# Kernel optimization log

Hardware: AMD Instinct MI355X
Metric: run time of the kernel (lower is better)

## Reference

```python
import jax, jax.numpy as jnp
import numpy as np

B = 128; Hm = 13; Wm = 13; P = Hm * Wm; D = 256; TC = 32; RH = 512; EPS = 1e-5
START_TILE = 31


def _ln(x, g, b):
    m = jnp.mean(x, -1, keepdims=True)
    v = jnp.mean((x - m) ** 2, -1, keepdims=True)
    return (x - m) * jax.lax.rsqrt(v + EPS) * g + b


def _gelu(x):
    return jax.nn.gelu(x, approximate=False)


def _fwd(target_map, map_vec, mv_w, mv_b, tile_emb, row_emb, col_emb, pos_w, pos_b,
         c1_w, c1_b, bn1_g, bn1_b, c2_w, c2_b, bn2_g, bn2_b, patch_fc_w, patch_fc_b,
         qkv_w, qkv_b, out_w, out_b, ln1_g, ln1_b, ff1_w, ff1_b, ff2_w, ff2_b,
         ln2_g, ln2_b, gru_wih, gru_whh, gru_bih, gru_bhh,
         fc1_w, fc1_b, fcln_g, fcln_b, fc2_w, fc2_b):
    Bn = map_vec.shape[0]
    ys = jnp.arange(P) // Wm
    xs = jnp.arange(P) % Wm
    d5 = jnp.arange(5)
    # map_vec projection [B,256]
    mv = map_vec @ mv_w.T + mv_b
    # positional embedding for all 169 positions: cat(row_emb[y], col_emb[x]) -> fusion
    pos = jnp.concatenate([row_emb[ys], col_emb[xs]], -1) @ pos_w.T + pos_b  # [P,256]
    # teacher-forced previous tile (use_self_probility=0 path)
    tflat = target_map.reshape(Bn, P)
    prev = jnp.concatenate([jnp.full((Bn, 1), START_TILE, tflat.dtype), tflat[:, :-1]], 1)
    te = tile_emb[prev]  # [B,P,256]
    # 5x5 causal patches: rows y-4..y, cols x-2..x+2, out-of-bounds + current/future-on-row masked
    padded = jnp.pad(target_map, ((0, 0), (4, 0), (2, 2)))  # [B,17,17]
    rows = ys[:, None] + d5
    cols = xs[:, None] + d5
    patch = padded[:, rows[:, :, None], cols[:, None, :]]  # [B,P,5,5]
    vr = (ys[:, None, None] - 4 + d5[None, :, None]) >= 0
    oc = xs[:, None, None] - 2 + d5[None, None, :]
    vc = (oc >= 0) & (oc < Wm)
    mask = (vr & vc)
    mask = mask.at[:, 4, 2:].set(False)  # zero current cell and the two to its right
    patch = jnp.where(mask[None], patch, 0)
    oh = jax.nn.one_hot(patch, TC, dtype=jnp.float32)  # [B,P,row,col,c]
    # torch: permute(0,3,2,1) transposes the spatial dims of the one-hot channels
    ch = jnp.transpose(oh, (0, 1, 4, 3, 2))  # [B,P,32,col,row]
    mch = jnp.broadcast_to(mask.astype(jnp.float32)[None, :, None], (Bn, P, 1, 5, 5))
    x = jnp.concatenate([ch, mch], 2).reshape(Bn * P, TC + 1, 5, 5)
    dn = ('NCHW', 'OIHW', 'NCHW')
    bnsc = 1.0 / np.sqrt(1.0 + EPS)  # eval BN with running mean 0 / var 1
    x = jax.lax.conv_general_dilated(x, c1_w, (1, 1), 'SAME', dimension_numbers=dn) + c1_b[None, :, None, None]
    x = _gelu(x * (bn1_g * bnsc)[None, :, None, None] + bn1_b[None, :, None, None])
    x = jax.lax.conv_general_dilated(x, c2_w, (1, 1), 'VALID', dimension_numbers=dn) + c2_b[None, :, None, None]
    x = _gelu(x * (bn2_g * bnsc)[None, :, None, None] + bn2_b[None, :, None, None])
    pf = x.reshape(Bn * P, 128 * 9) @ patch_fc_w.T + patch_fc_b  # [B*P,256]
    # fusion transformer over 4 tokens, batched across all 169 steps
    tok = jnp.stack([
        te.reshape(Bn * P, D),
        jnp.broadcast_to(mv[:, None], (Bn, P, D)).reshape(Bn * P, D),
        jnp.broadcast_to(pos[None], (Bn, P, D)).reshape(Bn * P, D),
        pf], 1)  # [B*P,4,256]
    h = tok
    for l in range(3):  # post-norm encoder layers, relu FFN, dropout=0 at eval
        qkv = h @ qkv_w[l].T + qkv_b[l]
        q, k, v = jnp.split(qkv, 3, -1)
        hd = lambda t: t.reshape(-1, 4, 2, 128).transpose(0, 2, 1, 3)  # 2 heads of 128
        q, k, v = hd(q), hd(k), hd(v)
        a = jax.nn.softmax(jnp.einsum('nhqd,nhkd->nhqk', q, k) / np.sqrt(128.0), -1)
        o = jnp.einsum('nhqk,nhkd->nhqd', a, v).transpose(0, 2, 1, 3).reshape(-1, 4, D)
        h = _ln(h + o @ out_w[l].T + out_b[l], ln1_g[l], ln1_b[l])
        ff = jax.nn.relu(h @ ff1_w[l].T + ff1_b[l]) @ ff2_w[l].T + ff2_b[l]
        h = _ln(h + ff, ln2_g[l], ln2_b[l])
    feat = h[:, 0].reshape(Bn, P, D).transpose(1, 0, 2)  # [P,B,256]
    # GRUCell recurrence over the 169 raster steps
    gi = feat @ gru_wih.T + gru_bih  # [P,B,1536]

    def step(hid, g):
        gh = hid @ gru_whh.T + gru_bhh
        ir, iz, inn = jnp.split(g, 3, -1)
        hr, hz, hn = jnp.split(gh, 3, -1)
        r = jax.nn.sigmoid(ir + hr)
        z = jax.nn.sigmoid(iz + hz)
        n = jnp.tanh(inn + r * hn)
        hid = (1 - z) * n + z * hid
        return hid, hid

    _, hs = jax.lax.scan(step, jnp.zeros((Bn, RH), jnp.float32), gi)  # [P,B,512]
    hs = hs.transpose(1, 0, 2)  # [B,P,512]
    y = _gelu(_ln(hs @ fc1_w.T + fc1_b, fcln_g, fcln_b))
    logits = y @ fc2_w.T + fc2_b  # [B,P,32]
    return logits.reshape(Bn, Hm, Wm, TC).transpose(0, 3, 1, 2)  # [B,32,13,13]


def setup_inputs() -> dict:
    key = jax.random.key(0)
    ks = jax.random.split(key, 24)
    r = lambda i, s: jax.random.normal(ks[i], s, jnp.float32) * 0.02
    return {
        'map_vec': jax.random.normal(ks[0], (B, 32), jnp.float32),
        'target_map': jax.random.randint(ks[1], (B, Hm, Wm), 0, TC, jnp.int32),
        'mv_w': r(2, (256, 32)), 'mv_b': jnp.zeros(256),
        'tile_emb': r(3, (32, 256)),
        'row_emb': r(4, (13, 256)), 'col_emb': r(5, (13, 256)),
        'pos_w': r(6, (256, 512)), 'pos_b': jnp.zeros(256),
        'c1_w': r(7, (64, 33, 3, 3)), 'c1_b': jnp.zeros(64),
        'bn1_g': jnp.ones(64), 'bn1_b': jnp.zeros(64),
        'c2_w': r(8, (128, 64, 3, 3)), 'c2_b': jnp.zeros(128),
        'bn2_g': jnp.ones(128), 'bn2_b': jnp.zeros(128),
        'patch_fc_w': r(9, (256, 1152)), 'patch_fc_b': jnp.zeros(256),
        'qkv_w': r(10, (3, 768, 256)), 'qkv_b': jnp.zeros((3, 768)),
        'out_w': r(11, (3, 256, 256)), 'out_b': jnp.zeros((3, 256)),
        'ln1_g': jnp.ones((3, 256)), 'ln1_b': jnp.zeros((3, 256)),
        'ff1_w': r(12, (3, 256, 256)), 'ff1_b': jnp.zeros((3, 256)),
        'ff2_w': r(13, (3, 256, 256)), 'ff2_b': jnp.zeros((3, 256)),
        'ln2_g': jnp.ones((3, 256)), 'ln2_b': jnp.zeros((3, 256)),
        'gru_wih': r(14, (1536, 256)), 'gru_whh': r(15, (1536, 512)),
        'gru_bih': jnp.zeros(1536), 'gru_bhh': jnp.zeros(1536),
        'fc1_w': r(16, (512, 512)), 'fc1_b': jnp.zeros(512),
        'fcln_g': jnp.ones(512), 'fcln_b': jnp.zeros(512),
        'fc2_w': r(17, (32, 512)), 'fc2_b': jnp.zeros(32),
    }


def reference(map_vec, target_map, mv_w, mv_b, tile_emb, row_emb, col_emb, pos_w, pos_b,
              c1_w, c1_b, bn1_g, bn1_b, c2_w, c2_b, bn2_g, bn2_b, patch_fc_w, patch_fc_b,
              qkv_w, qkv_b, out_w, out_b, ln1_g, ln1_b, ff1_w, ff1_b, ff2_w, ff2_b,
              ln2_g, ln2_b, gru_wih, gru_whh, gru_bih, gru_bhh,
              fc1_w, fc1_b, fcln_g, fcln_b, fc2_w, fc2_b):
    return _fwd(target_map, map_vec, mv_w, mv_b, tile_emb, row_emb, col_emb, pos_w, pos_b,
                c1_w, c1_b, bn1_g, bn1_b, c2_w, c2_b, bn2_g, bn2_b, patch_fc_w, patch_fc_b,
                qkv_w, qkv_b, out_w, out_b, ln1_g, ln1_b, ff1_w, ff1_b, ff2_w, ff2_b,
                ln2_g, ln2_b, gru_wih, gru_whh, gru_bih, gru_bhh,
                fc1_w, fc1_b, fcln_g, fcln_b, fc2_w, fc2_b)
```

## Files before the change

kernel.cpp:

```cpp
#include <hip/hip_runtime.h>
#include <hip/hip_bf16.h>

typedef unsigned short u16;
typedef unsigned char u8;
typedef unsigned int u32;
typedef __attribute__((ext_vector_type(8))) short bf16x8;
typedef __attribute__((ext_vector_type(4))) float f32x4;
typedef __attribute__((ext_vector_type(4))) unsigned int u32x4;

__device__ __forceinline__ float us2f(u16 u){ return __uint_as_float(((unsigned)u)<<16); }
__device__ __forceinline__ u16 f2us(float f){
  __hip_bfloat16 h = __float2bfloat16(f);
  union { __hip_bfloat16 b; u16 s; } cv; cv.b = h; return cv.s;
}
__device__ __forceinline__ float gelu_f(float v){ return 0.5f*v*(1.f+erff(v*0.70710678118654752f)); }
__device__ __forceinline__ float sigm_f(float v){ return 1.f/(1.f+expf(-v)); }

#define BNSC 0.9999950000374997f

struct PrepArgs {
  const float *qkv_w, *out_w, *ff1_w, *ff2_w, *g_wih, *fc1_w, *pf_w, *c2_w, *fc2_w, *fc2_b;
  const float *c1_w, *c1_b, *bn2_g;
  const float *map_vec, *mv_w, *mv_b, *row_e, *col_e, *pos_w, *pos_b;
  const int *tm;
  u16 *qkvw_d, *outw_d, *ff1w_d, *ff2w_d, *wihw_d, *fc1w_d, *pfw_d, *w2k_d, *fc2w_d;
  float *fc2b_d, *w1t_d, *t2_d, *s2_d, *mv_d, *pos_d;
  u8 *ecls_d;
  unsigned *bar;
};
#define SB_QKV 2304
#define SB_O   768
#define SB_WIH 1536
#define SB_FC1 1024
#define SB_PF  1152
#define SB_W2  288
#define SB_FC2 128
#define SB_W1T 72
#define SB_T2  1057
#define SB_MV  128
#define SB_POS 169
#define SB_EC  2113
#define PREP_GRID (1+SB_QKV+3*SB_O+SB_WIH+SB_FC1+SB_PF+SB_W2+SB_FC2+SB_W1T+SB_T2+SB_MV+SB_POS+SB_EC)

__global__ __launch_bounds__(256) void prep_kernel(PrepArgs a){
  int bb = blockIdx.x; const int tid = threadIdx.x;
  if (bb < 1){
    a.bar[tid] = 0u; a.bar[256+tid] = 0u;
    if (tid < 128) a.s2_d[tid] = a.bn2_g[tid]*BNSC;
    return;
  } bb -= 1;
  if (bb < SB_QKV){ int i = bb*256+tid; a.qkvw_d[i] = f2us(a.qkv_w[i]); return; } bb -= SB_QKV;
  if (bb < SB_O){ int i = bb*256+tid; a.outw_d[i] = f2us(a.out_w[i]); return; } bb -= SB_O;
  if (bb < SB_O){ int i = bb*256+tid; a.ff1w_d[i] = f2us(a.ff1_w[i]); return; } bb -= SB_O;
  if (bb < SB_O){ int i = bb*256+tid; a.ff2w_d[i] = f2us(a.ff2_w[i]); return; } bb -= SB_O;
  if (bb < SB_WIH){ int i = bb*256+tid; a.wihw_d[i] = f2us(a.g_wih[i]); return; } bb -= SB_WIH;
  if (bb < SB_FC1){ int i = bb*256+tid; a.fc1w_d[i] = f2us(a.fc1_w[i]); return; } bb -= SB_FC1;
  if (bb < SB_PF){
    int i = bb*256+tid;
    int o = i/1152, kp = i%1152, pos = kp>>7, c = kp&127;
    a.pfw_d[i] = f2us(a.pf_w[o*1152 + c*9 + pos]); return;
  } bb -= SB_PF;
  if (bb < SB_W2){
    int i = bb*256+tid;
    int o = i/576, k = i%576, tap = k>>6, ic = k&63, ty = tap/3, tx = tap%3;
    a.w2k_d[i] = f2us(a.c2_w[((o*64 + ic)*3 + ty)*3 + tx]); return;
  } bb -= SB_W2;
  if (bb < SB_FC2){
    int i = bb*256+tid;
    int o = i>>9, k = i&511;
    a.fc2w_d[i] = (o<32) ? f2us(a.fc2_w[o*512+k]) : (u16)0;
    if (i < 64) a.fc2b_d[i] = (i<32) ? a.fc2_b[i] : 0.f;
    return;
  } bb -= SB_FC2;
  if (bb < SB_W1T){
    int i = bb*256+tid;
    int c = i/576, r = i%576, tap = r>>6, o = r&63;
    a.w1t_d[i] = a.c1_w[(o*33 + c)*9 + tap]; return;
  } bb -= SB_W1T;
  if (bb < SB_T2){
    int i = bb*256+tid; if (i >= 169*25*64) return;
    int blk = i/64, o = i%64;
    int p = blk/25, op = blk%25, oy = op/5, ox = op%5;
    int yp = p/13, xp = p%13;
    float acc = a.c1_b[o];
    for (int dy=0; dy<3; dy++) for (int dx=0; dx<3; dx++){
      int Y = oy+dy-1, X = ox+dx-1;
      if (Y<0||Y>4||X<0||X>4) continue;
      int rr = yp + Y - 4, cc = xp + X - 2;
      bool m = (rr>=0) && (cc>=0) && (cc<13) && !(Y==4 && X>=2);
      if (m) acc += a.c1_w[(o*33 + 32)*9 + dy*3 + dx];
    }
    a.t2_d[((long)p*25 + op)*64 + o] = acc; return;
  } bb -= SB_T2;
  if (bb < SB_MV){
    int i = bb*256+tid;
    int bi = i>>8, o = i&255;
    float acc = a.mv_b[o];
    for (int k=0;k<32;k++) acc += a.map_vec[bi*32+k]*a.mv_w[o*32+k];
    a.mv_d[i] = acc; return;
  } bb -= SB_MV;
  if (bb < SB_POS){
    int i = bb*256+tid;
    int p = i>>8, o = i&255;
    int y = p/13, x = p%13;
    const float* wr = a.pos_w + o*512;
    float acc = a.pos_b[o];
    for (int k=0;k<256;k++) acc += a.row_e[y*256+k]*wr[k];
    for (int k=0;k<256;k++) acc += a.col_e[x*256+k]*wr[256+k];
    a.pos_d[i] = acc; return;
  } bb -= SB_POS;
  {
    int id = bb*256+tid; if (id >= 21632*25) return;
    int n = id/25, q = id%25, Y = q/5, X = q%5;
    int b = n/169, p = n%169, yp = p/13, xp = p%13;
    int rr = yp + X - 4, cc = xp + Y - 2;
    int val = 0;
    if (rr>=0 && cc>=0 && cc<13 && !(X==4 && Y>=2)) val = a.tm[b*169 + rr*13 + cc];
    a.ecls_d[id] = (u8)val;
  }
}

__global__ __launch_bounds__(256) void conv1_kernel(
    const u8* __restrict__ ec, const float* __restrict__ w1t, const float* __restrict__ t2,
    const float* __restrict__ bn1g, const float* __restrict__ bn1b, u16* __restrict__ c1out,
    int nbase){
  __shared__ __align__(16) u16 w1s[32*9*64];
  __shared__ u8 ecs[32*25];
  const int tid = threadIdx.x, nl0 = blockIdx.x*32;
  for (int i=tid; i<32*9*64; i+=256) w1s[i] = f2us(w1t[i]);
  for (int i=tid; i<32*25;   i+=256) ecs[i] = ec[((long)nbase + nl0)*25 + i];
  __syncthreads();
  const int grp = tid>>6, o = tid&63;
  const float s1 = bn1g[o]*BNSC, t1 = bn1b[o];
  for (int it = grp; it < 800; it += 4){
    const int nl = it/25, op = it%25, oy = op/5, ox = op%5;
    const int n = nbase + nl0 + nl, p = n%169;
    float acc = t2[((long)p*25 + op)*64 + o];
    #pragma unroll
    for (int dy=0; dy<3; dy++)
      #pragma unroll
      for (int dx=0; dx<3; dx++){
        int Y = oy+dy-1, X = ox+dx-1;
        if (Y>=0 && Y<5 && X>=0 && X<5){
          int e = ecs[nl*25 + Y*5 + X];
          acc += us2f(w1s[(e*9 + dy*3+dx)*64 + o]);
        }
      }
    c1out[((long)(nl0+nl)*25 + op)*64 + o] = f2us(gelu_f(acc*s1 + t1));
  }
}

template<int NT, int OM>
__global__ __launch_bounds__(256) void gemm_bt(
    const u16* A, long lda, const u16* __restrict__ W,
    const float* __restrict__ bias,
    float* outF, u16* outB, long ldc, int N, int K, int act,
    const u16* __restrict__ lbase, const float* __restrict__ lg, const float* __restrict__ lb){
  __shared__ __align__(16) u16 As[64][72];
  __shared__ __align__(16) u16 Ws[NT][64][72];
  const int tid = threadIdx.x, wv = tid>>6, lane = tid&63;
  const int quad = lane>>4, l16 = lane&15;
  const int bm = blockIdx.y, bn = blockIdx.x;
  f32x4 acc[NT*4];
  #pragma unroll
  for (int i=0;i<NT*4;i++) acc[i] = (f32x4){0.f,0.f,0.f,0.f};
  const int sm = tid>>2, sk = (tid&3)<<4;
  const long arow = (long)(bm*64 + sm)*lda;
  for (int kb = 0; kb < K; kb += 64){
    int4 a0 = *(const int4*)(A + arow + kb + sk);
    int4 a1 = *(const int4*)(A + arow + kb + sk + 8);
    *(int4*)&As[sm][sk]   = a0;  *(int4*)&As[sm][sk+8] = a1;
    #pragma unroll
    for (int wt=0; wt<NT; wt++){
      const long wrow = (long)(bn*(64*NT) + wt*64 + sm)*K;
      int4 w0 = *(const int4*)(W + wrow + kb + sk);
      int4 w1 = *(const int4*)(W + wrow + kb + sk + 8);
      *(int4*)&Ws[wt][sm][sk]   = w0;  *(int4*)&Ws[wt][sm][sk+8] = w1;
    }
    __syncthreads();
    #pragma unroll
    for (int ks = 0; ks < 64; ks += 32){
      bf16x8 af = *(const bf16x8*)(&As[wv*16 + l16][ks + quad*8]);
      #pragma unroll
      for (int wt=0; wt<NT; wt++)
        #pragma unroll
        for (int s=0; s<4; s++){
          bf16x8 bfv = *(const bf16x8*)(&Ws[wt][s*16 + l16][ks + quad*8]);
          acc[wt*4+s] = __builtin_amdgcn_mfma_f32_16x16x32_bf16(af, bfv, acc[wt*4+s], 0, 0, 0);
        }
    }
    __syncthreads();
  }
  const int mb = bm*64 + wv*16 + quad*4;
  if (OM == 2){
    #pragma unroll
    for (int wt=0; wt<NT; wt++)
      #pragma unroll
      for (int s=0; s<4; s++){
        const int n = wt*64 + s*16 + l16;
        const float bv = bias[n];
        #pragma unroll
        for (int r=0;r<4;r++)
          acc[wt*4+s][r] = acc[wt*4+s][r] + bv + us2f(lbase[(long)(mb+r)*N + n]);
      }
    float mean[4], rstd[4];
    #pragma unroll
    for (int r=0;r<4;r++){
      float s = 0.f;
      #pragma unroll
      for (int i=0;i<NT*4;i++) s += acc[i][r];
      s += __shfl_xor(s,1); s += __shfl_xor(s,2); s += __shfl_xor(s,4); s += __shfl_xor(s,8);
      mean[r] = s / N;
      float v = 0.f;
      #pragma unroll
      for (int i=0;i<NT*4;i++){ float d = acc[i][r]-mean[r]; v += d*d; }
      v += __shfl_xor(v,1); v += __shfl_xor(v,2); v += __shfl_xor(v,4); v += __shfl_xor(v,8);
      rstd[r] = rsqrtf(v/N + 1e-5f);
    }
    #pragma unroll
    for (int wt=0; wt<NT; wt++)
      #pragma unroll
      for (int s=0; s<4; s++){
        const int n = wt*64 + s*16 + l16;
        const float gv = lg[n], bvv = lb[n];
        #pragma unroll
        for (int r=0;r<4;r++)
          outB[(long)(mb+r)*ldc + n] = f2us((acc[wt*4+s][r]-mean[r])*rstd[r]*gv + bvv);
      }
    return;
  }
  #pragma unroll
  for (int wt=0; wt<NT; wt++)
    #pragma unroll
    for (int s=0; s<4; s++){
      const int n = bn*(64*NT) + wt*64 + s*16 + l16;
      const float bv = bias ? bias[n] : 0.f;
      #pragma unroll
      for (int r=0;r<4;r++){
        float v = acc[wt*4+s][r] + bv;
        if (act==1) v = fmaxf(v, 0.f);
        else if (act==2) v = gelu_f(v);
        if (OM == 1){
          const int m = mb + r, b = m/169, tt = m%169;
          const int gate = n>>9, cblk = (n>>4)&31, jl = n&15;
          outB[(((long)tt*32 + cblk)*3 + gate)*2048 + b*16 + jl] = f2us(v);
        } else if (OM == 3){
          if (n < 32){
            const int m = mb + r, t = m/128, b2 = m%128;
            outF[((long)b2*32 + n)*169 + t] = v;
          }
        } else {
          const long oo = (long)(mb + r)*ldc + n;
          if (outF) outF[oo] = v;
          if (outB) outB[oo] = f2us(v);
        }
      }
    }
}

__global__ __launch_bounds__(256) void gemm_conv2(
    const u16* __restrict__ C1, const u16* __restrict__ W,
    const float* __restrict__ bias, const float* __restrict__ scale, const float* __restrict__ shift,
    u16* __restrict__ outB){
  __shared__ __align__(16) u16 As[64][72];
  __shared__ __align__(16) u16 Ws[64][72];
  const int tid = threadIdx.x, wv = tid>>6, lane = tid&63;
  const int quad = lane>>4, l16 = lane&15;
  const int bm = blockIdx.y, bn = blockIdx.x;
  f32x4 acc[4];
  #pragma unroll
  for (int i=0;i<4;i++) acc[i] = (f32x4){0.f,0.f,0.f,0.f};
  const int sm = tid>>2, sk = (tid&3)<<4;
  const int g = bm*64 + sm, n_ = g/9, pos = g%9, py = pos/3, px = pos%3;
  const long wrow = (long)(bn*64 + sm)*576;
  for (int tap = 0; tap < 9; tap++){
    const int kb = tap*64;
    const long aoff = ((long)n_*25 + (py + tap/3)*5 + (px + tap%3))*64 + sk;
    int4 a0 = *(const int4*)(C1 + aoff);
    int4 a1 = *(const int4*)(C1 + aoff + 8);
    int4 w0 = *(const int4*)(W + wrow + kb + sk);
    int4 w1 = *(const int4*)(W + wrow + kb + sk + 8);
    *(int4*)&As[sm][sk]   = a0;  *(int4*)&As[sm][sk+8] = a1;
    *(int4*)&Ws[sm][sk]   = w0;  *(int4*)&Ws[sm][sk+8] = w1;
    __syncthreads();
    #pragma unroll
    for (int ks = 0; ks < 64; ks += 32){
      bf16x8 af = *(const bf16x8*)(&As[wv*16 + l16][ks + quad*8]);
      #pragma unroll
      for (int nt=0; nt<4; nt++){
        bf16x8 bfv = *(const bf16x8*)(&Ws[nt*16 + l16][ks + quad*8]);
        acc[nt] = __builtin_amdgcn_mfma_f32_16x16x32_bf16(af, bfv, acc[nt], 0, 0, 0);
      }
    }
    __syncthreads();
  }
  const int mb = bm*64 + wv*16 + quad*4;
  #pragma unroll
  for (int nt=0; nt<4; nt++){
    const int n = bn*64 + nt*16 + l16;
    const float bv = bias[n], sc = scale[n], sh = shift[n];
    #pragma unroll
    for (int r=0;r<4;r++){
      float v = (acc[nt][r] + bv)*sc + sh;
      outB[(long)(mb + r)*128 + n] = f2us(gelu_f(v));
    }
  }
}

__global__ void token_kernel(const int* __restrict__ tm, const float* __restrict__ te,
                             const float* __restrict__ mv, const float* __restrict__ pos,
                             u16* __restrict__ hB){
  const int n = blockIdx.x, k = threadIdx.x;
  const int b = n/169, p = n%169;
  const int prev = (p==0) ? 31 : tm[b*169 + p - 1];
  const long r0 = (long)n*1024;
  hB[r0 + k]        = f2us(te[prev*256 + k]);
  hB[r0 + 256 + k]  = f2us(mv[b*256 + k]);
  hB[r0 + 512 + k]  = f2us(pos[p*256 + k]);
}

__global__ __launch_bounds__(256) void attn_kernel(const u16* __restrict__ qkv, u16* o){
  const int n = blockIdx.x*4 + (threadIdx.x>>6);
  const int lane = threadIdx.x & 63;
  float qv[4][2][2], kv[4][2][2], vv[4][2][2];
  #pragma unroll
  for (int tok=0; tok<4; tok++){
    const long rb = (long)(n*4+tok)*768;
    #pragma unroll
    for (int h=0; h<2; h++){
      unsigned u;
      u = *(const unsigned*)(qkv + rb +        h*128 + 2*lane); qv[tok][h][0]=us2f(u&0xffff); qv[tok][h][1]=us2f(u>>16);
      u = *(const unsigned*)(qkv + rb + 256 +  h*128 + 2*lane); kv[tok][h][0]=us2f(u&0xffff); kv[tok][h][1]=us2f(u>>16);
      u = *(const unsigned*)(qkv + rb + 512 +  h*128 + 2*lane); vv[tok][h][0]=us2f(u&0xffff); vv[tok][h][1]=us2f(u>>16);
    }
  }
  float sc[2][4][4];
  #pragma unroll
  for (int h=0; h<2; h++)
    #pragma unroll
    for (int qt=0; qt<4; qt++)
      #pragma unroll
      for (int kt=0; kt<4; kt++){
        float p_ = qv[qt][h][0]*kv[kt][h][0] + qv[qt][h][1]*kv[kt][h][1];
        for (int off=32; off; off>>=1) p_ += __shfl_xor(p_, off);
        sc[h][qt][kt] = p_ * 0.08838834764831845f;
      }
  #pragma unroll
  for (int h=0; h<2; h++)
    #pragma unroll
    for (int qt=0; qt<4; qt++){
      float m = fmaxf(fmaxf(sc[h][qt][0],sc[h][qt][1]),fmaxf(sc[h][qt][2],sc[h][qt][3]));
      float s = 0.f;
      #pragma unroll
      for (int kt=0; kt<4; kt++){ sc[h][qt][kt] = expf(sc[h][qt][kt]-m); s += sc[h][qt][kt]; }
      float inv = 1.f/s;
      #pragma unroll
      for (int kt=0; kt<4; kt++) sc[h][qt][kt] *= inv;
    }
  #pragma unroll
  for (int qt=0; qt<4; qt++)
    #pragma unroll
    for (int h=0; h<2; h++){
      float o0=0.f, o1=0.f;
      #pragma unroll
      for (int kt=0; kt<4; kt++){ o0 += sc[h][qt][kt]*vv[kt][h][0]; o1 += sc[h][qt][kt]*vv[kt][h][1]; }
      unsigned u = (unsigned)f2us(o0) | ((unsigned)f2us(o1)<<16);
      *(unsigned*)(o + (long)(n*4+qt)*256 + h*128 + 2*lane) = u;
    }
}

template<int NPL>
__global__ __launch_bounds__(256) void ln_kernel(
    const u16* __restrict__ delta, const u16* __restrict__ base,
    const float* __restrict__ g, const float* __restrict__ b,
    u16* __restrict__ out, int do_gelu){
  const int D = NPL*64;
  const int row = blockIdx.x*4 + (threadIdx.x>>6);
  const int lane = threadIdx.x & 63;
  const long ro = (long)row*D;
  float x[NPL];
  float s = 0.f;
  #pragma unroll
  for (int i=0;i<NPL;i++){
    float v = us2f(delta[ro + i*64 + lane]);
    if (base) v += us2f(base[ro + i*64 + lane]);
    x[i] = v; s += v;
  }
  for (int off=32; off; off>>=1) s += __shfl_xor(s, off);
  const float mean = s / D;
  float var = 0.f;
  #pragma unroll
  for (int i=0;i<NPL;i++){ float dd = x[i]-mean; var += dd*dd; }
  for (int off=32; off; off>>=1) var += __shfl_xor(var, off);
  const float rs = rsqrtf(var/D + 1e-5f);
  #pragma unroll
  for (int i=0;i<NPL;i++){
    float y = (x[i]-mean)*rs*g[i*64+lane] + b[i*64+lane];
    if (do_gelu) y = gelu_f(y);
    out[ro + i*64 + lane] = f2us(y);
  }
}

__global__ __launch_bounds__(256) void gru_kernel(
    const u16* __restrict__ gix, const float* __restrict__ whh,
    const float* __restrict__ bhh, u16* __restrict__ hx, u16* __restrict__ hs,
    unsigned* __restrict__ bar){
  __shared__ __align__(16) u16 Wl[48][520];
  __shared__ __align__(16) u16 hbuf[2048];
  const int c = blockIdx.x, tid = threadIdx.x;
  const int wv = tid>>6, lane = tid&63, quad = lane>>4, l16 = lane&15;
  for (int idx = tid; idx < 48*512; idx += 256){
    int g = idx >> 9, k = idx & 511;
    int gate = g >> 4, jl = g & 15;
    Wl[g][k] = f2us(whh[((gate<<9) + (c<<4) + jl)*512 + k]);
  }
  const int j = (c<<4) + l16;
  const float bh_r = bhh[j], bh_z = bhh[512+j], bh_n = bhh[1024+j];
  __syncthreads();
  float hold[2][4] = {{0.f,0.f,0.f,0.f},{0.f,0.f,0.f,0.f}};
  const int jlo = (quad&1)*8, jhiadd = quad>>1;
  for (int t=0; t<169; t++){
    const u16* gbase = gix + ((long)t*32 + c)*3*2048;
    float gr_[2][4], gz_[2][4], gn_[2][4];
    #pragma unroll
    for (int mt=0; mt<2; mt++)
      #pragma unroll
      for (int r=0; r<4; r++){
        const int b = (2*wv+mt)*16 + quad*4 + r;
        gr_[mt][r] = us2f(gbase[       b*16 + l16]);
        gz_[mt][r] = us2f(gbase[2048 + b*16 + l16]);
        gn_[mt][r] = us2f(gbase[4096 + b*16 + l16]);
      }
    if (t>0){
      if (tid < 32){
        const u32* fp = bar + tid*16;
        u32 v;
        do {
          asm volatile("global_load_dword %0, %1, off sc0 sc1" : "=v"(v) : "v"(fp));
          asm volatile("s_waitcnt vmcnt(0)" ::: "memory");
        } while ((int)v < t);
      }
      __syncthreads();
    }
    f32x4 acc[2][3];
    #pragma unroll
    for (int mt=0; mt<2; mt++)
      #pragma unroll
      for (int g3=0; g3<3; g3++) acc[mt][g3] = (f32x4){0.f,0.f,0.f,0.f};
    if (t>0){
      const long tb = (long)(t-1)*65536;
      const int b0 = (2*wv+0)*16 + l16, b1 = (2*wv+1)*16 + l16;
      bf16x8 av0[16], av1[16];
      #pragma unroll
      for (int ii=0; ii<16; ii++){
        const long off = tb + (long)(ii*2 + jhiadd)*2048 + jlo;
        const u16* p0 = hx + off + b0*16;
        const u16* p1 = hx + off + b1*16;
        asm volatile("global_load_dwordx4 %0, %1, off sc0 sc1" : "=v"(av0[ii]) : "v"(p0));
        asm volatile("global_load_dwordx4 %0, %1, off sc0 sc1" : "=v"(av1[ii]) : "v"(p1));
      }
      asm volatile("s_waitcnt vmcnt(0)" ::: "memory");
      #pragma unroll
      for (int ii=0; ii<16; ii++){
        asm volatile("" : "+v"(av0[ii]));
        asm volatile("" : "+v"(av1[ii]));
      }
      #pragma unroll
      for (int ii=0; ii<16; ii++){
        const int ks = ii*32;
        #pragma unroll
        for (int g3=0; g3<3; g3++){
          bf16x8 bfv = *(const bf16x8*)(&Wl[g3*16 + l16][ks + quad*8]);
          acc[0][g3] = __builtin_amdgcn_mfma_f32_16x16x32_bf16(av0[ii], bfv, acc[0][g3], 0,0,0);
          acc[1][g3] = __builtin_amdgcn_mfma_f32_16x16x32_bf16(av1[ii], bfv, acc[1][g3], 0,0,0);
        }
      }
    }
    u16 hbv[2][4];
    #pragma unroll
    for (int mt=0; mt<2; mt++)
      #pragma unroll
      for (int r=0; r<4; r++){
        const int b = (2*wv+mt)*16 + quad*4 + r;
        float rr = sigm_f(gr_[mt][r] + acc[mt][0][r] + bh_r);
        float zz = sigm_f(gz_[mt][r] + acc[mt][1][r] + bh_z);
        float nn = tanhf (gn_[mt][r] + rr*(acc[mt][2][r] + bh_n));
        float h = (1.f-zz)*nn + zz*hold[mt][r];
        hold[mt][r] = h;
        hbv[mt][r] = f2us(h);
        hbuf[b*16 + l16] = hbv[mt][r];
      }
    __syncthreads();
    {
      u16* dst = hx + (long)t*65536 + c*2048 + tid*8;
      u32x4 val = *(const u32x4*)((const u32*)hbuf + tid*4);
      asm volatile("global_store_dwordx4 %0, %1, off sc0 sc1" :: "v"(dst), "v"(val) : "memory");
    }
    asm volatile("s_waitcnt vmcnt(0)" ::: "memory");
    __syncthreads();
    if (tid==0){
      u32 tv = (u32)(t+1);
      const u32* fp = bar + c*16;
      asm volatile("global_store_dword %0, %1, off sc0 sc1" :: "v"(fp), "v"(tv) : "memory");
    }
    #pragma unroll
    for (int mt=0; mt<2; mt++)
      #pragma unroll
      for (int r=0; r<4; r++){
        const int b = (2*wv+mt)*16 + quad*4 + r;
        hs[((long)(t*128 + b))*512 + j] = hbv[mt][r];
      }
  }
}

extern "C" void kernel_launch(void* const* d_in, const int* in_sizes, int n_in,
                              void* d_out, int out_size, void* d_ws, size_t ws_size,
                              hipStream_t stream){
  (void)in_sizes; (void)n_in; (void)out_size;
  const float* map_vec = (const float*)d_in[0];
  const int*   tm      = (const int*)  d_in[1];
  const float* mv_w  = (const float*)d_in[2];
  const float* mv_b  = (const float*)d_in[3];
  const float* te    = (const float*)d_in[4];
  const float* row_e = (const float*)d_in[5];
  const float* col_e = (const float*)d_in[6];
  const float* pos_w = (const float*)d_in[7];
  const float* pos_b = (const float*)d_in[8];
  const float* c1_w  = (const float*)d_in[9];
  const float* c1_b  = (const float*)d_in[10];
  const float* bn1_g = (const float*)d_in[11];
  const float* bn1_b = (const float*)d_in[12];
  const float* c2_w  = (const float*)d_in[13];
  const float* c2_b  = (const float*)d_in[14];
  const float* bn2_g = (const float*)d_in[15];
  const float* bn2_b = (const float*)d_in[16];
  const float* pf_w  = (const float*)d_in[17];
  const float* pf_b  = (const float*)d_in[18];
  const float* qkv_w = (const float*)d_in[19];
  const float* qkv_b = (const float*)d_in[20];
  const float* out_w = (const float*)d_in[21];
  const float* out_b = (const float*)d_in[22];
  const float* ln1_g = (const float*)d_in[23];
  const float* ln1_b = (const float*)d_in[24];
  const float* ff1_w = (const float*)d_in[25];
  const float* ff1_b = (const float*)d_in[26];
  const float* ff2_w = (const float*)d_in[27];
  const float* ff2_b = (const float*)d_in[28];
  const float* ln2_g = (const float*)d_in[29];
  const float* ln2_b = (const float*)d_in[30];
  const float* g_wih = (const float*)d_in[31];
  const float* g_whh = (const float*)d_in[32];
  const float* g_bih = (const float*)d_in[33];
  const float* g_bhh = (const float*)d_in[34];
  const float* fc1_w = (const float*)d_in[35];
  const float* fc1_b = (const float*)d_in[36];
  const float* fln_g = (const float*)d_in[37];
  const float* fln_b = (const float*)d_in[38];
  const float* fc2_w = (const float*)d_in[39];
  const float* fc2_b = (const float*)d_in[40];

  char* ws = (char*)d_ws;
  constexpr size_t O_BAR  = 0;
  constexpr size_t O_QKVW = 2048;
  constexpr size_t O_OUTW = O_QKVW + 1179648;
  constexpr size_t O_FF1W = O_OUTW + 393216;
  constexpr size_t O_FF2W = O_FF1W + 393216;
  constexpr size_t O_WIHW = O_FF2W + 393216;
  constexpr size_t O_FC1W = O_WIHW + 786432;
  constexpr size_t O_PFW  = O_FC1W + 524288;
  constexpr size_t O_W2K  = O_PFW  + 589824;
  constexpr size_t O_FC2W = O_W2K  + 147456;
  constexpr size_t O_FC2B = O_FC2W + 65536;
  constexpr size_t O_W1T  = O_FC2B + 256;
  constexpr size_t O_T2   = O_W1T  + 73728;
  constexpr size_t O_S2   = O_T2   + 1081600;
  constexpr size_t O_MV   = O_S2   + 512;
  constexpr size_t O_POS  = O_MV   + 131072;
  constexpr size_t O_ECLS = O_POS  + 173056;
  constexpr size_t O_R0   = ((O_ECLS + 540800 + 255)/256)*256;
  constexpr size_t R0_SZ  = 44302336;
  constexpr size_t O_R1   = O_R0 + R0_SZ;
  constexpr size_t R1_SZ  = 44302336;
  constexpr size_t O_R2   = O_R1 + R1_SZ;
  constexpr size_t R2_SZ  = 33226752;
  constexpr size_t ARENA_END = O_R2 + R2_SZ;
  if (ws_size < ARENA_END) return;
  const size_t O_HB    = O_R0;
  const size_t O_HX    = O_R0;
  const size_t O_HS    = O_R0 + 22151168;
  const size_t O_C1OUT = O_R1;
  const size_t O_OBUF  = O_R1;
  const size_t O_GIX   = O_R1;
  const size_t O_Y1    = O_R1;
  const size_t O_YB    = O_R1 + 22151168;
  const size_t O_C2OUT = O_R2;
  const size_t O_QKVC  = O_R2;

  PrepArgs pa;
  pa.qkv_w=qkv_w; pa.out_w=out_w; pa.ff1_w=ff1_w; pa.ff2_w=ff2_w; pa.g_wih=g_wih;
  pa.fc1_w=fc1_w; pa.pf_w=pf_w; pa.c2_w=c2_w; pa.fc2_w=fc2_w; pa.fc2_b=fc2_b;
  pa.c1_w=c1_w; pa.c1_b=c1_b; pa.bn2_g=bn2_g;
  pa.map_vec=map_vec; pa.mv_w=mv_w; pa.mv_b=mv_b; pa.row_e=row_e; pa.col_e=col_e;
  pa.pos_w=pos_w; pa.pos_b=pos_b; pa.tm=tm;
  pa.qkvw_d=(u16*)(ws+O_QKVW); pa.outw_d=(u16*)(ws+O_OUTW); pa.ff1w_d=(u16*)(ws+O_FF1W);
  pa.ff2w_d=(u16*)(ws+O_FF2W); pa.wihw_d=(u16*)(ws+O_WIHW); pa.fc1w_d=(u16*)(ws+O_FC1W);
  pa.pfw_d=(u16*)(ws+O_PFW); pa.w2k_d=(u16*)(ws+O_W2K); pa.fc2w_d=(u16*)(ws+O_FC2W);
  pa.fc2b_d=(float*)(ws+O_FC2B); pa.w1t_d=(float*)(ws+O_W1T); pa.t2_d=(float*)(ws+O_T2);
  pa.s2_d=(float*)(ws+O_S2); pa.mv_d=(float*)(ws+O_MV); pa.pos_d=(float*)(ws+O_POS);
  pa.ecls_d=(u8*)(ws+O_ECLS); pa.bar=(unsigned*)(ws+O_BAR);
  prep_kernel<<<PREP_GRID, 256, 0, stream>>>(pa);

  token_kernel<<<21632, 256, 0, stream>>>(tm, te, (const float*)(ws+O_MV), (const float*)(ws+O_POS),
      (u16*)(ws+O_HB));

  for (int cc = 0; cc < 2; cc++){
    const int nbase = cc*10816;
    conv1_kernel<<<338, 256, 0, stream>>>((const u8*)(ws+O_ECLS), (const float*)(ws+O_W1T),
        (const float*)(ws+O_T2), bn1_g, bn1_b, (u16*)(ws+O_C1OUT), nbase);
    gemm_conv2<<<dim3(2,1521), 256, 0, stream>>>((const u16*)(ws+O_C1OUT), (const u16*)(ws+O_W2K),
        c2_b, (const float*)(ws+O_S2), bn2_b, (u16*)(ws+O_C2OUT));
    gemm_bt<4,0><<<dim3(1,169), 256, 0, stream>>>((const u16*)(ws+O_C2OUT), 1152, (const u16*)(ws+O_PFW),
        pf_b, nullptr, (u16*)(ws+O_HB) + (size_t)nbase*1024 + 768, 1024, 256, 1152, 0,
        nullptr, nullptr, nullptr);
  }

  for (int l=0; l<3; l++){
    for (int cc = 0; cc < 4; cc++){
      gemm_bt<4,0><<<dim3(3,338), 256, 0, stream>>>((const u16*)(ws+O_HB) + (size_t)cc*21632*256, 256,
          (const u16*)(ws+O_QKVW) + (size_t)l*768*256, qkv_b + l*768,
          nullptr, (u16*)(ws+O_QKVC), 768, 768, 256, 0, nullptr, nullptr, nullptr);
      attn_kernel<<<1352, 256, 0, stream>>>((const u16*)(ws+O_QKVC),
          (u16*)(ws+O_OBUF) + (size_t)cc*5408*4*256);
    }
    gemm_bt<4,2><<<dim3(1,1352), 256, 0, stream>>>((const u16*)(ws+O_OBUF), 256,
        (const u16*)(ws+O_OUTW) + (size_t)l*256*256, out_b + l*256,
        nullptr, (u16*)(ws+O_HB), 256, 256, 256, 0,
        (const u16*)(ws+O_HB), ln1_g + l*256, ln1_b + l*256);
    gemm_bt<4,0><<<dim3(1,1352), 256, 0, stream>>>((const u16*)(ws+O_HB), 256,
        (const u16*)(ws+O_FF1W) + (size_t)l*256*256, ff1_b + l*256,
        nullptr, (u16*)(ws+O_OBUF), 256, 256, 256, 1, nullptr, nullptr, nullptr);
    gemm_bt<4,2><<<dim3(1,1352), 256, 0, stream>>>((const u16*)(ws+O_OBUF), 256,
        (const u16*)(ws+O_FF2W) + (size_t)l*256*256, ff2_b + l*256,
        nullptr, (u16*)(ws+O_HB), 256, 256, 256, 0,
        (const u16*)(ws+O_HB), ln2_g + l*256, ln2_b + l*256);
  }

  gemm_bt<4,1><<<dim3(6,338), 256, 0, stream>>>((const u16*)(ws+O_HB), 1024, (const u16*)(ws+O_WIHW),
      g_bih, nullptr, (u16*)(ws+O_GIX), 1536, 1536, 256, 0, nullptr, nullptr, nullptr);
  gru_kernel<<<32, 256, 0, stream>>>((const u16*)(ws+O_GIX), g_whh, g_bhh,
      (u16*)(ws+O_HX), (u16*)(ws+O_HS), (unsigned*)(ws+O_BAR));

  gemm_bt<4,0><<<dim3(2,338), 256, 0, stream>>>((const u16*)(ws+O_HS), 512, (const u16*)(ws+O_FC1W),
      fc1_b, nullptr, (u16*)(ws+O_Y1), 512, 512, 512, 0, nullptr, nullptr, nullptr);
  ln_kernel<8><<<5408, 256, 0, stream>>>((const u16*)(ws+O_Y1), nullptr, fln_g, fln_b,
      (u16*)(ws+O_YB), 1);
  gemm_bt<1,3><<<dim3(1,338), 256, 0, stream>>>((const u16*)(ws+O_YB), 512, (const u16*)(ws+O_FC2W),
      (const float*)(ws+O_FC2B), (float*)d_out, nullptr, 64, 64, 512, 0, nullptr, nullptr, nullptr);
}
```

Measured before the change: 2.910 ms.

## Split GRU recurrence across four batch groups with 128 blocks

The persistent GRU kernel now runs 128 blocks of 128 threads instead of 32 blocks of 256. Each block handles one 16-column hidden slice for a 32-row batch group, and the barrier only waits on the 32 blocks of the same batch group, since batch groups are independent. The input-gate GEMM output and the hidden-state exchange buffer are re-laid out so each block reads contiguous, batch-group-local data. The aim is to spread the serial 169-step recurrence over more CUs and cut per-step work and sync fan-in. In exchange each block stages the full Whh slice in LDS, so weight loading is duplicated four times.

Result: no change. 2.887 ms (-0.8%).

```diff
diff --git a/kernel.cpp b/kernel.cpp
--- a/kernel.cpp
+++ b/kernel.cpp
@@ -242,8 +242,8 @@
         else if (act==2) v = gelu_f(v);
         if (OM == 1){
           const int m = mb + r, b = m/169, tt = m%169;
-          const int gate = n>>9, cblk = (n>>4)&31, jl = n&15;
-          outB[(((long)tt*32 + cblk)*3 + gate)*2048 + b*16 + jl] = f2us(v);
+          const int g = n>>9, j = n&511, cs = j>>4, jl = j&15, bg = b>>5, bl = b&31;
+          outB[((((long)tt*4 + bg)*32 + cs)*48 + g*16 + jl)*32 + bl] = f2us(v);
         } else if (OM == 3){
           if (n < 32){
             const int m = mb + r, t = m/128, b2 = m%128;
@@ -401,39 +401,37 @@
   }
 }
 
-__global__ __launch_bounds__(256) void gru_kernel(
-    const u16* __restrict__ gix, const float* __restrict__ whh,
+__global__ __launch_bounds__(128) void gru_kernel(
+    const u16* __restrict__ giz, const float* __restrict__ whh,
     const float* __restrict__ bhh, u16* __restrict__ hx, u16* __restrict__ hs,
     unsigned* __restrict__ bar){
   __shared__ __align__(16) u16 Wl[48][520];
-  __shared__ __align__(16) u16 hbuf[2048];
+  __shared__ __align__(16) u16 hbuf[32][16];
   const int c = blockIdx.x, tid = threadIdx.x;
+  const int bg = c>>5, cs = c&31;
   const int wv = tid>>6, lane = tid&63, quad = lane>>4, l16 = lane&15;
-  for (int idx = tid; idx < 48*512; idx += 256){
-    int g = idx >> 9, k = idx & 511;
-    int gate = g >> 4, jl = g & 15;
-    Wl[g][k] = f2us(whh[((gate<<9) + (c<<4) + jl)*512 + k]);
-  }
-  const int j = (c<<4) + l16;
+  for (int idx = tid; idx < 48*512; idx += 128){
+    int rr = idx >> 9, k = idx & 511;
+    int gate = rr >> 4, jl = rr & 15;
+    Wl[rr][k] = f2us(whh[((gate<<9) + (cs<<4) + jl)*512 + k]);
+  }
+  const int j = (cs<<4) + l16;
   const float bh_r = bhh[j], bh_z = bhh[512+j], bh_n = bhh[1024+j];
   __syncthreads();
-  float hold[2][4] = {{0.f,0.f,0.f,0.f},{0.f,0.f,0.f,0.f}};
-  const int jlo = (quad&1)*8, jhiadd = quad>>1;
+  float hold[4] = {0.f,0.f,0.f,0.f};
   for (int t=0; t<169; t++){
-    const u16* gbase = gix + ((long)t*32 + c)*3*2048;
-    float gr_[2][4], gz_[2][4], gn_[2][4];
-    #pragma unroll
-    for (int mt=0; mt<2; mt++)
-      #pragma unroll
-      for (int r=0; r<4; r++){
-        const int b = (2*wv+mt)*16 + quad*4 + r;
-        gr_[mt][r] = us2f(gbase[       b*16 + l16]);
-        gz_[mt][r] = us2f(gbase[2048 + b*16 + l16]);
-        gn_[mt][r] = us2f(gbase[4096 + b*16 + l16]);
-      }
+    const u16* gbase = giz + (((long)t*4 + bg)*32 + cs)*1536;
+    float gr_[4], gz_[4], gn_[4];
+    #pragma unroll
+    for (int r=0; r<4; r++){
+      const int bl = wv*16 + quad*4 + r;
+      gr_[r] = us2f(gbase[(0*16 + l16)*32 + bl]);
+      gz_[r] = us2f(gbase[(1*16 + l16)*32 + bl]);
+      gn_[r] = us2f(gbase[(2*16 + l16)*32 + bl]);
+    }
     if (t>0){
       if (tid < 32){
-        const u32* fp = bar + tid*16;
+        const u32* fp = bar + (bg*32 + tid)*4;
         u32 v;
         do {
           asm volatile("global_load_dword %0, %1, off sc0 sc1" : "=v"(v) : "v"(fp));
@@ -442,74 +440,60 @@
       }
       __syncthreads();
     }
-    f32x4 acc[2][3];
-    #pragma unroll
-    for (int mt=0; mt<2; mt++)
-      #pragma unroll
-      for (int g3=0; g3<3; g3++) acc[mt][g3] = (f32x4){0.f,0.f,0.f,0.f};
+    f32x4 acc[3];
+    #pragma unroll
+    for (int g3=0; g3<3; g3++) acc[g3] = (f32x4){0.f,0.f,0.f,0.f};
     if (t>0){
-      const long tb = (long)(t-1)*65536;
-      const int b0 = (2*wv+0)*16 + l16, b1 = (2*wv+1)*16 + l16;
-      bf16x8 av0[16], av1[16];
-      #pragma unroll
-      for (int ii=0; ii<16; ii++){
-        const long off = tb + (long)(ii*2 + jhiadd)*2048 + jlo;
-        const u16* p0 = hx + off + b0*16;
-        const u16* p1 = hx + off + b1*16;
-        asm volatile("global_load_dwordx4 %0, %1, off sc0 sc1" : "=v"(av0[ii]) : "v"(p0));
-        asm volatile("global_load_dwordx4 %0, %1, off sc0 sc1" : "=v"(av1[ii]) : "v"(p1));
+      const long tb = ((long)(t-1)*4 + bg)*16384;
+      const int bl = wv*16 + l16;
+      bf16x8 av[16];
+      #pragma unroll
+      for (int ks=0; ks<16; ks++){
+        const u16* p0 = hx + tb + bl*512 + ks*32 + quad*8;
+        asm volatile("global_load_dwordx4 %0, %1, off sc0 sc1" : "=v"(av[ks]) : "v"(p0));
       }
       asm volatile("s_waitcnt vmcnt(0)" ::: "memory");
       #pragma unroll
-      for (int ii=0; ii<16; ii++){
-        asm volatile("" : "+v"(av0[ii]));
-        asm volatile("" : "+v"(av1[ii]));
-      }
-      #pragma unroll
-      for (int ii=0; ii<16; ii++){
-        const int ks = ii*32;
+      for (int ks=0; ks<16; ks++) asm volatile("" : "+v"(av[ks]));
+      #pragma unroll
+      for (int ks=0; ks<16; ks++){
         #pragma unroll
         for (int g3=0; g3<3; g3++){
-          bf16x8 bfv = *(const bf16x8*)(&Wl[g3*16 + l16][ks + quad*8]);
-          acc[0][g3] = __builtin_amdgcn_mfma_f32_16x16x32_bf16(av0[ii], bfv, acc[0][g3], 0,0,0);
-          acc[1][g3] = __builtin_amdgcn_mfma_f32_16x16x32_bf16(av1[ii], bfv, acc[1][g3], 0,0,0);
+          bf16x8 bfv = *(const bf16x8*)(&Wl[g3*16 + l16][ks*32 + quad*8]);
+          acc[g3] = __builtin_amdgcn_mfma_f32_16x16x32_bf16(av[ks], bfv, acc[g3], 0,0,0);
         }
       }
     }
-    u16 hbv[2][4];
-    #pragma unroll
-    for (int mt=0; mt<2; mt++)
-      #pragma unroll
-      for (int r=0; r<4; r++){
-        const int b = (2*wv+mt)*16 + quad*4 + r;
-        float rr = sigm_f(gr_[mt][r] + acc[mt][0][r] + bh_r);
-        float zz = sigm_f(gz_[mt][r] + acc[mt][1][r] + bh_z);
-        float nn = tanhf (gn_[mt][r] + rr*(acc[mt][2][r] + bh_n));
-        float h = (1.f-zz)*nn + zz*hold[mt][r];
-        hold[mt][r] = h;
-        hbv[mt][r] = f2us(h);
-        hbuf[b*16 + l16] = hbv[mt][r];
-      }
+    u16 hbv[4];
+    #pragma unroll
+    for (int r=0; r<4; r++){
+      float rr = sigm_f(gr_[r] + acc[0][r] + bh_r);
+      float zz = sigm_f(gz_[r] + acc[1][r] + bh_z);
+      float nn = tanhf (gn_[r] + rr*(acc[2][r] + bh_n));
+      float h = (1.f-zz)*nn + zz*hold[r];
+      hold[r] = h;
+      hbv[r] = f2us(h);
+      hbuf[wv*16 + quad*4 + r][l16] = hbv[r];
+    }
     __syncthreads();
-    {
-      u16* dst = hx + (long)t*65536 + c*2048 + tid*8;
-      u32x4 val = *(const u32x4*)((const u32*)hbuf + tid*4);
+    if (tid < 64){
+      const int bl = tid>>1, half = tid&1;
+      u16* dst = hx + ((long)t*4 + bg)*16384 + bl*512 + cs*16 + half*8;
+      u32x4 val = *(const u32x4*)(&hbuf[bl][half*8]);
       asm volatile("global_store_dwordx4 %0, %1, off sc0 sc1" :: "v"(dst), "v"(val) : "memory");
     }
     asm volatile("s_waitcnt vmcnt(0)" ::: "memory");
     __syncthreads();
     if (tid==0){
       u32 tv = (u32)(t+1);
-      const u32* fp = bar + c*16;
+      const u32* fp = bar + c*4;
       asm volatile("global_store_dword %0, %1, off sc0 sc1" :: "v"(fp), "v"(tv) : "memory");
     }
     #pragma unroll
-    for (int mt=0; mt<2; mt++)
-      #pragma unroll
-      for (int r=0; r<4; r++){
-        const int b = (2*wv+mt)*16 + quad*4 + r;
-        hs[((long)(t*128 + b))*512 + j] = hbv[mt][r];
-      }
+    for (int r=0; r<4; r++){
+      const int b = bg*32 + wv*16 + quad*4 + r;
+      hs[((long)(t*128 + b))*512 + j] = hbv[r];
+    }
   }
 }
 
@@ -590,7 +574,7 @@
   const size_t O_HS    = O_R0 + 22151168;
   const size_t O_C1OUT = O_R1;
   const size_t O_OBUF  = O_R1;
-  const size_t O_GIX   = O_R1;
+  const size_t O_GIZ   = O_R1;
   const size_t O_Y1    = O_R1;
   const size_t O_YB    = O_R1 + 22151168;
   const size_t O_C2OUT = O_R2;
@@ -646,8 +630,8 @@
   }
 
   gemm_bt<4,1><<<dim3(6,338), 256, 0, stream>>>((const u16*)(ws+O_HB), 1024, (const u16*)(ws+O_WIHW),
-      g_bih, nullptr, (u16*)(ws+O_GIX), 1536, 1536, 256, 0, nullptr, nullptr, nullptr);
-  gru_kernel<<<32, 256, 0, stream>>>((const u16*)(ws+O_GIX), g_whh, g_bhh,
+      g_bih, nullptr, (u16*)(ws+O_GIZ), 1536, 1536, 256, 0, nullptr, nullptr, nullptr);
+  gru_kernel<<<128, 128, 0, stream>>>((const u16*)(ws+O_GIZ), g_whh, g_bhh,
       (u16*)(ws+O_HX), (u16*)(ws+O_HS), (unsigned*)(ws+O_BAR));
 
   gemm_bt<4,0><<<dim3(2,338), 256, 0, stream>>>((const u16*)(ws+O_HS), 512, (const u16*)(ws+O_FC1W),
```
